# Kernel tuning notes

Measured on AMD Instinct MI355X. Metric: run time of the kernel, lower is better.

Reference implementation:

```python
import jax, jax.numpy as jnp
import numpy as np

B, M, N, P, H = 8192, 4, 2, 2, 128
D5 = M * 5            # FC5 output = m * in_mult_KNet
D2H = (H + H) * 40    # FC2 hidden = d_input_FC2 * out_mult_KNet


def _lin(x, W, b):
    return x @ W.T + b


def _gru(x, h, Wih, Whh, bih, bhh):
    # PyTorch GRU cell math (single layer, single step)
    gi = x @ Wih.T + bih   # [B, 3H]
    gh = h @ Whh.T + bhh   # [B, 3H]
    ir, iz, inn = jnp.split(gi, 3, axis=-1)
    hr, hz, hn = jnp.split(gh, 3, axis=-1)
    r = jax.nn.sigmoid(ir + hr)
    z = jax.nn.sigmoid(iz + hz)
    n = jnp.tanh(inn + r * hn)
    return (1.0 - z) * n + z * h


def setup_inputs() -> dict:
    key = jax.random.key(0)
    ks = iter(jax.random.split(key, 64))
    rn = lambda *s: jax.random.normal(next(ks), s, dtype=jnp.float32)
    sc = lambda d: np.float32(1.0 / np.sqrt(d))
    inp = {
        'y': rn(B, N, 1), 'u': rn(B, P, 1), 'm1x_post': rn(B, M, 1),
        'h_Q': jnp.zeros((B, H), jnp.float32),
        'h_Sigma': jnp.zeros((B, H), jnp.float32),
        'h_S': jnp.zeros((B, H), jnp.float32),
        'F_mat': jnp.eye(M, dtype=jnp.float32) + 0.1 * rn(M, M),
        'G_mat': 0.1 * rn(M, P),
        'H_mat': 0.5 * rn(N, M),
        'innov_logit': jnp.float32(0.0),
        'W_fc5': rn(D5, M) * sc(M), 'b_fc5': rn(D5) * 0.01,
        'Wih_Q': rn(3 * H, D5) * sc(H), 'Whh_Q': rn(3 * H, H) * sc(H),
        'bih_Q': rn(3 * H) * 0.01, 'bhh_Q': rn(3 * H) * 0.01,
        'Wih_Sig': rn(3 * H, H) * sc(H), 'Whh_Sig': rn(3 * H, H) * sc(H),
        'bih_Sig': rn(3 * H) * 0.01, 'bhh_Sig': rn(3 * H) * 0.01,
        'W_fc1': rn(N * N, H) * sc(H), 'b_fc1': rn(N * N) * 0.01,
        'W_fc7': rn(N, N) * sc(N), 'b_fc7': rn(N) * 0.01,
        'Wih_S': rn(3 * H, N * N + N) * sc(H), 'Whh_S': rn(3 * H, H) * sc(H),
        'bih_S': rn(3 * H) * 0.01, 'bhh_S': rn(3 * H) * 0.01,
        'W_fc2a': rn(D2H, 2 * H) * sc(2 * H), 'b_fc2a': rn(D2H) * 0.01,
        'W_fc2b': rn(N * M, D2H) * sc(D2H), 'b_fc2b': rn(N * M) * 0.01,
        'W_fc3': rn(M * M, H + N * M) * sc(H + N * M), 'b_fc3': rn(M * M) * 0.01,
        'W_fc4': rn(H, H + M * M) * sc(H + M * M), 'b_fc4': rn(H) * 0.01,
    }
    return inp


def reference(y, u, m1x_post, h_Q, h_Sigma, h_S, F_mat, G_mat, H_mat, innov_logit,
              W_fc5, b_fc5, Wih_Q, Whh_Q, bih_Q, bhh_Q,
              Wih_Sig, Whh_Sig, bih_Sig, bhh_Sig,
              W_fc1, b_fc1, W_fc7, b_fc7,
              Wih_S, Whh_S, bih_S, bhh_S,
              W_fc2a, b_fc2a, W_fc2b, b_fc2b,
              W_fc3, b_fc3, W_fc4, b_fc4):
    relu = jax.nn.relu
    # --- step_prior: linear system model f(x,u)=Fx+Gu, h(x)=Hx (no normalization) ---
    x_post = m1x_post[..., 0]                      # [B, M]
    x_prior = x_post @ F_mat.T + u[..., 0] @ G_mat.T
    y_pred = x_prior @ H_mat.T                     # [B, N]
    dy = y[..., 0] - y_pred                        # innovation [B, N]
    # --- KGain_step (dropout = identity at inference) ---
    out5 = relu(_lin(x_prior, W_fc5, b_fc5))       # [B, 20]
    hQ_new = _gru(out5, h_Q, Wih_Q, Whh_Q, bih_Q, bhh_Q)
    hSig = _gru(hQ_new, h_Sigma, Wih_Sig, Whh_Sig, bih_Sig, bhh_Sig)
    out1 = relu(_lin(hSig, W_fc1, b_fc1))          # [B, n^2]
    out7 = relu(_lin(dy, W_fc7, b_fc7))            # [B, n]
    hS_new = _gru(jnp.concatenate([out1, out7], -1), h_S, Wih_S, Whh_S, bih_S, bhh_S)
    in2 = jnp.concatenate([hSig, hS_new], -1)      # [B, 256]
    out2 = _lin(relu(_lin(in2, W_fc2a, b_fc2a)), W_fc2b, b_fc2b)  # KG flat [B, n*m]
    out3 = relu(_lin(jnp.concatenate([hS_new, out2], -1), W_fc3, b_fc3))
    hSig_new = relu(_lin(jnp.concatenate([hSig, out3], -1), W_fc4, b_fc4))
    # --- posterior update ---
    KG = out2.reshape(B, M, N)
    gamma = jax.nn.sigmoid(innov_logit)
    inov = gamma * jnp.einsum('bmn,bn->bm', KG, dy)
    m1x_posterior = (x_prior + inov)[..., None]    # [B, M, 1]
    return m1x_posterior, hQ_new, hSig_new, hS_new
```

## Files before the change

### kernel.cpp

```cpp
#include <hip/hip_runtime.h>
#include <hip/hip_bf16.h>

typedef __attribute__((ext_vector_type(8))) short bf16x8;
typedef __attribute__((ext_vector_type(4))) float f32x4;
typedef __attribute__((ext_vector_type(4))) short s16x4;
typedef __attribute__((ext_vector_type(4))) float f32v4;
typedef unsigned short u16;
typedef unsigned int u32;

__device__ inline u16 f2b(float f){ __hip_bfloat16 b = __float2bfloat16(f); return __builtin_bit_cast(unsigned short, b); }
__device__ inline float b2f(u16 u){ unsigned int x = ((unsigned int)u)<<16; return __builtin_bit_cast(float, x); }
__device__ inline float sigm(float x){ return 1.f/(1.f+__expf(-x)); }
__device__ inline float tanhfast(float x){ float e = __expf(2.f*x); return 1.f - 2.f/(e+1.f); }

__device__ inline f32x4 mfma16(bf16x8 a, bf16x8 b, f32x4 c){
  return __builtin_amdgcn_mfma_f32_16x16x32_bf16(a, b, c, 0, 0, 0);
}

__device__ __forceinline__ void in2t_store(u16* t, int row, int col, u16 v){
  int rt = row>>4, kk = col>>5, khi = (col>>3)&3, e = col&7;
  t[(size_t)(rt*8+kk)*512 + (khi*16 + (row&15))*8 + e] = v;
}
__device__ __forceinline__ s16x4 in2t_load4(const u16* t, int row, int col){
  int rt = row>>4, kk = col>>5, khi = (col>>3)&3, e = col&7;
  return *(const s16x4*)(t + (size_t)(rt*8+kk)*512 + (khi*16 + (row&15))*8 + e);
}

struct CVA {
  const float *w2a, *w2b, *wihQ, *whhQ, *wihSg, *whhSg, *wihS, *whhS, *wfc3, *wfc4;
  u16 *waB, *wbB, *wihQp, *whhQb, *wihSgB, *whhSgB, *wihSp, *whhSb, *wfc3p, *wfc4p;
};

__global__ __launch_bounds__(256) void kconv(CVA a){
  int id = blockIdx.x*256 + threadIdx.x;
  if (id < 2621440){
    int t  = id >> 12;
    int r  = id & 4095;
    int kk = r >> 9;
    int l  = (r >> 3) & 63;
    int e  = id & 7;
    int col = t*16 + (l & 15);
    int k   = kk*32 + (l >> 4)*8 + e;
    a.waB[id] = f2b(a.w2a[col*256 + k]);
    return;
  }
  id -= 2621440;
  if (id < 163840){
    int s = id >> 9;
    int r = id & 511;
    int l = r >> 3;
    int e = r & 7;
    int o = l & 15;
    int q = (l >> 4)*8 + e;
    int k = s*32 + (q&1)*16 + (q>>1);
    a.wbB[id] = (o < 8) ? f2b(a.w2b[o*10240 + k]) : (u16)0;
    return;
  }
  id -= 163840;
  if (id < 12288){ int j=id>>5, k=id&31; a.wihQp[id] = (k<20)? f2b(a.wihQ[j*20+k]) : (u16)0; return; }
  id -= 12288;
  if (id < 49152){ a.whhQb[id] = f2b(a.whhQ[id]); return; }
  id -= 49152;
  if (id < 49152){ a.wihSgB[id] = f2b(a.wihSg[id]); return; }
  id -= 49152;
  if (id < 49152){ a.whhSgB[id] = f2b(a.whhSg[id]); return; }
  id -= 49152;
  if (id < 12288){ int j=id>>5, k=id&31; a.wihSp[id] = (k<6)? f2b(a.wihS[j*6+k]) : (u16)0; return; }
  id -= 12288;
  if (id < 49152){ a.whhSb[id] = f2b(a.whhS[id]); return; }
  id -= 49152;
  if (id < 2560){ int j=id/160, k=id%160; a.wfc3p[id] = (k<136)? f2b(a.wfc3[j*136+k]) : (u16)0; return; }
}

__global__ __launch_bounds__(256) void kconv_fc4(const float* wfc4, u16* wfc4p){
  int id = blockIdx.x*256 + threadIdx.x;
  if (id < 20480){ int j=id/160, k=id%160; wfc4p[id] = (k<144)? f2b(wfc4[j*144+k]) : (u16)0; }
}

template<int KX, int LDX, bool SOUT, bool GB16, bool GF32>
__device__ __forceinline__ void gru_step(
    const u16* sX, const u16* sH,
    const u16* __restrict__ Wih, const int ldwih, const u16* __restrict__ Whh,
    const float* __restrict__ bih, const float* __restrict__ bhh,
    float* __restrict__ gOutF, u16* sOut,
    u16* __restrict__ in2T, int row0, int colOff)
{
  const int tid = threadIdx.x;
  const int w = tid>>6, lane = tid&63, c = lane&15, khi = lane>>4;
  for (int nn=0; nn<2; ++nn){
    const int n = w*2+nn;
    const int j = n*16 + c;
    const float bir=bih[j], biz=bih[128+j], bin=bih[256+j];
    const float bhr=bhh[j], bhz=bhh[128+j], bhn=bhh[256+j];
    bf16x8 BX0[KX], BX1[KX], BX2[KX], BH0[4], BH1[4], BH2[4];
    #pragma unroll
    for (int kk=0;kk<KX;++kk){
      const u16* p = Wih + j*ldwih + kk*32 + khi*8;
      BX0[kk] = *(const bf16x8*)(p);
      BX1[kk] = *(const bf16x8*)(p + 128*ldwih);
      BX2[kk] = *(const bf16x8*)(p + 256*ldwih);
    }
    #pragma unroll
    for (int kk=0;kk<4;++kk){
      const u16* p = Whh + j*128 + kk*32 + khi*8;
      BH0[kk] = *(const bf16x8*)(p);
      BH1[kk] = *(const bf16x8*)(p + 128*128);
      BH2[kk] = *(const bf16x8*)(p + 256*128);
    }
    #pragma unroll
    for (int m=0;m<2;++m){
      f32x4 ir={0,0,0,0}, iz={0,0,0,0}, inx={0,0,0,0};
      f32x4 hr={0,0,0,0}, hz={0,0,0,0}, hn={0,0,0,0};
      #pragma unroll
      for (int kk=0;kk<KX;++kk){
        bf16x8 A = *(const bf16x8*)(sX + (m*16+c)*LDX + kk*32 + khi*8);
        ir  = mfma16(A, BX0[kk], ir);
        iz  = mfma16(A, BX1[kk], iz);
        inx = mfma16(A, BX2[kk], inx);
      }
      #pragma unroll
      for (int kk=0;kk<4;++kk){
        bf16x8 A = *(const bf16x8*)(sH + (m*16+c)*136 + kk*32 + khi*8);
        hr = mfma16(A, BH0[kk], hr);
        hz = mfma16(A, BH1[kk], hz);
        hn = mfma16(A, BH2[kk], hn);
      }
      #pragma unroll
      for (int e=0;e<4;++e){
        int r = m*16 + khi*4 + e;
        float rg = sigm(ir[e]+hr[e]+bir+bhr);
        float zg = sigm(iz[e]+hz[e]+biz+bhz);
        float ng = tanhfast(inx[e]+bin + rg*(hn[e]+bhn));
        float hold = b2f(sH[r*136 + j]);
        float hv = (1.f-zg)*ng + zg*hold;
        if (GF32) gOutF[r*128 + j] = hv;
        if (SOUT) sOut[r*136 + j] = f2b(hv);
        if (GB16) in2t_store(in2T, row0 + r, colOff + j, f2b(hv));
      }
    }
  }
}

struct K1A {
  const float *y,*u,*m1x,*hQ,*hSg,*hS,*F,*G,*Hm,*W5,*b5,
              *bihQ,*bhhQ,*bihSg,*bhhSg,*W1,*b1,*W7,*b7,*bihS,*bhhS;
  const u16 *wihQp,*whhQ,*wihSg,*whhSg,*wihSp,*whhS;
  float *outHQ,*outHS,*xp,*dy;
  u16 *in2T;
};

__device__ __forceinline__ void load_h_tile(u16* dst, const float* src, int row0){
  const int tid = threadIdx.x;
  #pragma unroll
  for (int i=0;i<4;++i){
    int f4 = tid + i*256;
    int r = f4>>5, c4 = f4&31;
    f32v4 v = *(const f32v4*)(src + (row0+r)*128 + c4*4);
    s16x4 o;
    o[0]=(short)f2b(v[0]); o[1]=(short)f2b(v[1]);
    o[2]=(short)f2b(v[2]); o[3]=(short)f2b(v[3]);
    *(s16x4*)(dst + r*136 + c4*4) = o;
  }
}

__global__ __launch_bounds__(256) void k1(K1A a){
  __shared__ u16 sX[32*40];
  __shared__ u16 sH[32*136];
  __shared__ u16 sXL[32*136];
  __shared__ u16 sSig[32*136];
  __shared__ float sDY[64];
  const int row0 = blockIdx.x*32;
  const int tid = threadIdx.x;

  load_h_tile(sH, a.hQ, row0);
  if (tid < 32){
    int r = tid, row = row0 + r;
    float xpost[4], uu[2], xpr[4];
    #pragma unroll
    for (int i=0;i<4;++i) xpost[i]=a.m1x[row*4+i];
    uu[0]=a.u[row*2]; uu[1]=a.u[row*2+1];
    #pragma unroll
    for (int i=0;i<4;++i){
      float s=0.f;
      #pragma unroll
      for (int jj=0;jj<4;++jj) s += a.F[i*4+jj]*xpost[jj];
      #pragma unroll
      for (int jj=0;jj<2;++jj) s += a.G[i*2+jj]*uu[jj];
      xpr[i]=s; a.xp[row*4+i]=s;
    }
    #pragma unroll
    for (int nn2=0;nn2<2;++nn2){
      float s=0.f;
      #pragma unroll
      for (int jj=0;jj<4;++jj) s += a.Hm[nn2*4+jj]*xpr[jj];
      float d = a.y[row*2+nn2]-s;
      a.dy[row*2+nn2]=d; sDY[r*2+nn2]=d;
    }
    #pragma unroll
    for (int o=0;o<20;++o){
      float s=a.b5[o];
      #pragma unroll
      for (int k=0;k<4;++k) s += a.W5[o*4+k]*xpr[k];
      sX[r*40+o]=f2b(fmaxf(s,0.f));
    }
    for (int o=20;o<40;++o) sX[r*40+o]=0;
  }
  __syncthreads();
  gru_step<1,40,true,false,true>(sX, sH, a.wihQp, 32, a.whhQ, a.bihQ, a.bhhQ,
                                 a.outHQ + row0*128, sXL, nullptr, 0, 0);
  __syncthreads();
  load_h_tile(sH, a.hSg, row0);
  __syncthreads();
  gru_step<4,136,true,true,false>(sXL, sH, a.wihSg, 128, a.whhSg, a.bihSg, a.bhhSg,
                                  nullptr, sSig, a.in2T, row0, 0);
  __syncthreads();
  if (tid < 128){
    int r = tid>>2, o = tid&3;
    float s = a.b1[o];
    for (int k=0;k<128;++k) s += a.W1[o*128+k]*b2f(sSig[r*136+k]);
    sX[r*40+o] = f2b(fmaxf(s,0.f));
  } else if (tid < 192){
    int t = tid-128; int r=t>>1, o=t&1;
    float s = a.b7[o] + a.W7[o*2]*sDY[r*2] + a.W7[o*2+1]*sDY[r*2+1];
    sX[r*40+4+o] = f2b(fmaxf(s,0.f));
  }
  for (int i=tid;i<32*26;i+=256){ int r=i/26, cc=6+(i%26); sX[r*40+cc]=0; }
  load_h_tile(sH, a.hS, row0);
  __syncthreads();
  gru_step<1,40,false,true,true>(sX, sH, a.wihSp, 32, a.whhS, a.bihS, a.bhhS,
                                 a.outHS + row0*128, nullptr, a.in2T, row0, 128);
}

struct K2A {
  const u16 *waB, *wbB, *in2T;
  const float *b2a;
  float *parts;
};

__global__ __launch_bounds__(512) void k2(K2A a){
  __shared__ u16 sA[128*256];
  __shared__ u16 sHw[8][16*40];
  const int bid = blockIdx.x;
  const int rb = bid>>3, ch = bid&7;
  const int tid = threadIdx.x;
  const int wid = tid>>6, lane = tid&63, c = lane&15, khi = lane>>4;
  const int wr = wid>>2, wc = wid&3;

  {
    const s16x4* src = (const s16x4*)(a.in2T + (size_t)rb*32768);
    s16x4* dst = (s16x4*)sA;
    #pragma unroll
    for (int i=0;i<16;++i) dst[tid + i*512] = src[tid + i*512];
  }
  __syncthreads();

  f32x4 C2[4];
  #pragma unroll
  for (int m=0;m<4;++m) C2[m] = (f32x4){0,0,0,0};
  u16* hw = &sHw[wid][0];

  for (int it=0; it<10; ++it){
    const int colb = ch*1280 + it*128 + wc*32;
    const int t0 = colb>>4;
    f32x4 C1[4][2];
    #pragma unroll
    for (int m=0;m<4;++m){ C1[m][0]=(f32x4){0,0,0,0}; C1[m][1]=(f32x4){0,0,0,0}; }
    #pragma unroll
    for (int kk=0;kk<8;++kk){
      bf16x8 Bf0 = *(const bf16x8*)(a.waB + (size_t)(t0*8+kk)*512 + lane*8);
      bf16x8 Bf1 = *(const bf16x8*)(a.waB + (size_t)((t0+1)*8+kk)*512 + lane*8);
      #pragma unroll
      for (int m=0;m<4;++m){
        bf16x8 Ar = *(const bf16x8*)(sA + (size_t)((wr*4+m)*8+kk)*512 + lane*8);
        C1[m][0] = mfma16(Ar, Bf0, C1[m][0]);
        C1[m][1] = mfma16(Ar, Bf1, C1[m][1]);
      }
    }
    bf16x8 B2 = *(const bf16x8*)(a.wbB + (size_t)(colb>>5)*512 + lane*8);
    const float bias0 = a.b2a[colb + c];
    const float bias1 = a.b2a[colb + 16 + c];
    #pragma unroll
    for (int m=0;m<4;++m){
      #pragma unroll
      for (int e=0;e<4;++e){
        float v0 = fmaxf(C1[m][0][e]+bias0, 0.f);
        float v1 = fmaxf(C1[m][1][e]+bias1, 0.f);
        u32 w = (u32)f2b(v0) | ((u32)f2b(v1)<<16);
        *(u32*)(hw + (khi*4+e)*40 + 2*c) = w;
      }
      bf16x8 A2 = *(const bf16x8*)(hw + c*40 + khi*8);
      C2[m] = mfma16(A2, B2, C2[m]);
    }
  }
  __syncthreads();
  float* sRed = (float*)sA;
  if (c < 8){
    #pragma unroll
    for (int m=0;m<4;++m)
      #pragma unroll
      for (int e=0;e<4;++e)
        sRed[wid*512 + (m*16+khi*4+e)*8 + c] = C2[m][e];
  }
  __syncthreads();
  #pragma unroll
  for (int i=tid;i<1024;i+=512){
    int r=i>>3, o=i&7;
    int band=r>>6, rl=r&63;
    float s=0.f;
    #pragma unroll
    for (int w2=0;w2<4;++w2) s += sRed[(band*4+w2)*512 + rl*8 + o];
    a.parts[(size_t)ch*65536 + (size_t)(rb*128+r)*8 + o] = s;
  }
}

struct K3A {
  const float *parts;
  const float *b2b, *bfc3, *bfc4, *xp, *dy, *innov;
  const u16 *in2T, *wfc3p, *wfc4p;
  float *outPost, *outHSig;
};

__global__ __launch_bounds__(256) void k3(K3A a){
  __shared__ u16 sA[64*168];
  __shared__ u16 sX4[64*168];
  __shared__ float sOut2[64*8];
  const int row0 = blockIdx.x*64;
  const int tid = threadIdx.x;
  for (int i=tid;i<512;i+=256){
    int r=i>>3, o=i&7, row=row0+r;
    float s = a.b2b[o];
    #pragma unroll
    for (int chv=0;chv<8;++chv) s += a.parts[chv*65536 + row*8 + o];
    sOut2[i]=s;
    sA[r*168+128+o]=f2b(s);
  }
  for (int i=tid;i<2048;i+=256){
    int r=i>>5, c4=i&31;
    int row = row0 + r, col = c4*4;
    *(s16x4*)(sX4 + r*168 + col) = in2t_load4(a.in2T, row, col);
    *(s16x4*)(sA  + r*168 + col) = in2t_load4(a.in2T, row, 128 + col);
  }
  for (int i=tid;i<64*6;i+=256){
    int r=i/6, c4=i%6;
    *(s16x4*)(sA + r*168 + 136 + c4*4) = (s16x4){0,0,0,0};
  }
  for (int i=tid;i<64*4;i+=256){
    int r=i>>2, c4=i&3;
    *(s16x4*)(sX4 + r*168 + 144 + c4*4) = (s16x4){0,0,0,0};
  }
  __syncthreads();
  {
    int r = tid>>2, m = tid&3, row = row0+r;
    float g = 1.f/(1.f+__expf(-a.innov[0]));
    float d0 = a.dy[row*2], d1 = a.dy[row*2+1];
    float k0 = sOut2[r*8+m*2], k1 = sOut2[r*8+m*2+1];
    a.outPost[row*4+m] = a.xp[row*4+m] + g*(k0*d0+k1*d1);
  }
  const int w = tid>>6, lane = tid&63, c = lane&15, khi = lane>>4;
  {
    f32x4 C3 = {0,0,0,0};
    #pragma unroll
    for (int kk=0;kk<5;++kk){
      bf16x8 A  = *(const bf16x8*)(sA + (w*16+c)*168 + kk*32 + khi*8);
      bf16x8 Bf = *(const bf16x8*)(a.wfc3p + c*160 + kk*32 + khi*8);
      C3 = mfma16(A,Bf,C3);
    }
    float bj = a.bfc3[c];
    #pragma unroll
    for (int e=0;e<4;++e){
      int r = w*16 + khi*4 + e;
      sX4[r*168 + 128 + c] = f2b(fmaxf(C3[e]+bj, 0.f));
    }
  }
  __syncthreads();
  for (int nn=0;nn<2;++nn){
    int j = (w*2+nn)*16 + c;
    bf16x8 Bf[5];
    #pragma unroll
    for (int kk=0;kk<5;++kk) Bf[kk] = *(const bf16x8*)(a.wfc4p + j*160 + kk*32 + khi*8);
    float bj = a.bfc4[j];
    #pragma unroll
    for (int m=0;m<4;++m){
      f32x4 C = {0,0,0,0};
      #pragma unroll
      for (int kk=0;kk<5;++kk){
        bf16x8 A = *(const bf16x8*)(sX4 + (m*16+c)*168 + kk*32 + khi*8);
        C = mfma16(A, Bf[kk], C);
      }
      #pragma unroll
      for (int e=0;e<4;++e){
        int r = m*16 + khi*4 + e;
        a.outHSig[(row0+r)*128 + j] = fmaxf(C[e]+bj, 0.f);
      }
    }
  }
}

extern "C" void kernel_launch(void* const* d_in, const int* in_sizes, int n_in,
                              void* d_out, int out_size, void* d_ws, size_t ws_size,
                              hipStream_t stream){
  const float* y    = (const float*)d_in[0];
  const float* u    = (const float*)d_in[1];
  const float* m1x  = (const float*)d_in[2];
  const float* hQ   = (const float*)d_in[3];
  const float* hSg  = (const float*)d_in[4];
  const float* hS   = (const float*)d_in[5];
  const float* F    = (const float*)d_in[6];
  const float* G    = (const float*)d_in[7];
  const float* Hm   = (const float*)d_in[8];
  const float* innov= (const float*)d_in[9];
  const float* W5   = (const float*)d_in[10];
  const float* b5   = (const float*)d_in[11];
  const float* WihQ = (const float*)d_in[12];
  const float* WhhQ = (const float*)d_in[13];
  const float* bihQ = (const float*)d_in[14];
  const float* bhhQ = (const float*)d_in[15];
  const float* WihSg= (const float*)d_in[16];
  const float* WhhSg= (const float*)d_in[17];
  const float* bihSg= (const float*)d_in[18];
  const float* bhhSg= (const float*)d_in[19];
  const float* W1   = (const float*)d_in[20];
  const float* b1   = (const float*)d_in[21];
  const float* W7   = (const float*)d_in[22];
  const float* b7   = (const float*)d_in[23];
  const float* WihS = (const float*)d_in[24];
  const float* WhhS = (const float*)d_in[25];
  const float* bihS = (const float*)d_in[26];
  const float* bhhS = (const float*)d_in[27];
  const float* W2a  = (const float*)d_in[28];
  const float* b2a  = (const float*)d_in[29];
  const float* W2b  = (const float*)d_in[30];
  const float* b2b  = (const float*)d_in[31];
  const float* W3   = (const float*)d_in[32];
  const float* b3   = (const float*)d_in[33];
  const float* W4   = (const float*)d_in[34];
  const float* b4   = (const float*)d_in[35];

  const size_t WS_NEEDED = 12547072;
  if (ws_size < WS_NEEDED) return;

  char* ws = (char*)d_ws;
  u16*  waB   = (u16*)(ws + 0);
  u16*  wbB   = (u16*)(ws + 5242880);
  u16*  in2T  = (u16*)(ws + 5570560);
  float* parts= (float*)(ws + 9764864);
  float* xp   = (float*)(ws + 11862016);
  float* dyb  = (float*)(ws + 11993088);
  u16* wihQp  = (u16*)(ws + 12058624);
  u16* whhQb  = (u16*)(ws + 12083200);
  u16* wihSgB = (u16*)(ws + 12181504);
  u16* whhSgB = (u16*)(ws + 12279808);
  u16* wihSp  = (u16*)(ws + 12378112);
  u16* whhSb  = (u16*)(ws + 12402688);
  u16* wfc3p  = (u16*)(ws + 12500992);
  u16* wfc4p  = (u16*)(ws + 12506112);

  float* outF    = (float*)d_out;
  float* outPost = outF;
  float* outHQ   = outF + 32768;
  float* outHSig = outF + 32768 + 1048576;
  float* outHS   = outF + 32768 + 2*1048576;

  CVA cv{W2a, W2b, WihQ, WhhQ, WihSg, WhhSg, WihS, WhhS, W3, W4,
         waB, wbB, wihQp, whhQb, wihSgB, whhSgB, wihSp, whhSb, wfc3p, wfc4p};
  kconv<<<dim3(11834), dim3(256), 0, stream>>>(cv);
  kconv_fc4<<<dim3(80), dim3(256), 0, stream>>>(W4, wfc4p);

  K1A a1{y,u,m1x,hQ,hSg,hS,F,G,Hm,W5,b5,bihQ,bhhQ,bihSg,bhhSg,W1,b1,W7,b7,bihS,bhhS,
         wihQp,whhQb,wihSgB,whhSgB,wihSp,whhSb,
         outHQ,outHS,xp,dyb,in2T};
  k1<<<dim3(256), dim3(256), 0, stream>>>(a1);

  K2A a2{waB, wbB, in2T, b2a, parts};
  k2<<<dim3(512), dim3(512), 0, stream>>>(a2);

  K3A a3{parts, b2b, b3, b4, xp, dyb, innov, in2T, wfc3p, wfc4p, outPost, outHSig};
  k3<<<dim3(128), dim3(256), 0, stream>>>(a3);
}
```

Before: 100.8 us.

## Vectorize weight conversion, merge fc4 conversion, MFMA fc1, halve k3 tile

The weight-conversion kernel now handles eight elements per thread with float4 loads for the large FC2 weights, and the separate fc4 conversion launch is folded into it. This cuts thread count and one launch. In k1 the scalar 128-length fc1 dot products are replaced by a single-wave MFMA, and the zero-fill is spread across the remaining waves. k3 now processes 32 rows per block over 256 blocks to improve occupancy, at the cost of idle waves during the fc3 stage.

```diff
diff --git a/kernel.cpp b/kernel.cpp
--- a/kernel.cpp
+++ b/kernel.cpp
@@ -33,30 +33,44 @@
 
 __global__ __launch_bounds__(256) void kconv(CVA a){
   int id = blockIdx.x*256 + threadIdx.x;
-  if (id < 2621440){
-    int t  = id >> 12;
-    int r  = id & 4095;
-    int kk = r >> 9;
-    int l  = (r >> 3) & 63;
-    int e  = id & 7;
-    int col = t*16 + (l & 15);
-    int k   = kk*32 + (l >> 4)*8 + e;
-    a.waB[id] = f2b(a.w2a[col*256 + k]);
+  if (id < 327680){
+    int g = id >> 6;
+    int l = id & 63;
+    int col = (g>>3)*16 + (l & 15);
+    int k0  = (g&7)*32 + (l >> 4)*8;
+    const float* p = a.w2a + (size_t)col*256 + k0;
+    f32v4 v0 = *(const f32v4*)p;
+    f32v4 v1 = *(const f32v4*)(p+4);
+    s16x4 o0, o1;
+    #pragma unroll
+    for (int e=0;e<4;++e){ o0[e]=(short)f2b(v0[e]); o1[e]=(short)f2b(v1[e]); }
+    u16* d = a.waB + (size_t)g*512 + l*8;
+    *(s16x4*)d = o0; *(s16x4*)(d+4) = o1;
     return;
   }
-  id -= 2621440;
-  if (id < 163840){
-    int s = id >> 9;
-    int r = id & 511;
-    int l = r >> 3;
-    int e = r & 7;
+  id -= 327680;
+  if (id < 20480){
+    int l = id & 63;
     int o = l & 15;
-    int q = (l >> 4)*8 + e;
-    int k = s*32 + (q&1)*16 + (q>>1);
-    a.wbB[id] = (o < 8) ? f2b(a.w2b[o*10240 + k]) : (u16)0;
+    int b = (l >> 4)*4;
+    u16* d = a.wbB + (size_t)id*8;
+    if (o < 8){
+      int s = id >> 6;
+      const float* p = a.w2b + (size_t)o*10240 + s*32;
+      f32v4 v0 = *(const f32v4*)(p + b);
+      f32v4 v1 = *(const f32v4*)(p + 16 + b);
+      s16x4 o0, o1;
+      o0[0]=(short)f2b(v0[0]); o0[1]=(short)f2b(v1[0]);
+      o0[2]=(short)f2b(v0[1]); o0[3]=(short)f2b(v1[1]);
+      o1[0]=(short)f2b(v0[2]); o1[1]=(short)f2b(v1[2]);
+      o1[2]=(short)f2b(v0[3]); o1[3]=(short)f2b(v1[3]);
+      *(s16x4*)d = o0; *(s16x4*)(d+4) = o1;
+    } else {
+      *(s16x4*)d = (s16x4){0,0,0,0}; *(s16x4*)(d+4) = (s16x4){0,0,0,0};
+    }
     return;
   }
-  id -= 163840;
+  id -= 20480;
   if (id < 12288){ int j=id>>5, k=id&31; a.wihQp[id] = (k<20)? f2b(a.wihQ[j*20+k]) : (u16)0; return; }
   id -= 12288;
   if (id < 49152){ a.whhQb[id] = f2b(a.whhQ[id]); return; }
@@ -70,11 +84,8 @@
   if (id < 49152){ a.whhSb[id] = f2b(a.whhS[id]); return; }
   id -= 49152;
   if (id < 2560){ int j=id/160, k=id%160; a.wfc3p[id] = (k<136)? f2b(a.wfc3[j*136+k]) : (u16)0; return; }
-}
-
-__global__ __launch_bounds__(256) void kconv_fc4(const float* wfc4, u16* wfc4p){
-  int id = blockIdx.x*256 + threadIdx.x;
-  if (id < 20480){ int j=id/160, k=id%160; wfc4p[id] = (k<144)? f2b(wfc4[j*144+k]) : (u16)0; }
+  id -= 2560;
+  if (id < 20480){ int j=id/160, k=id%160; a.wfc4p[id] = (k<144)? f2b(a.wfc4[j*144+k]) : (u16)0; return; }
 }
 
 template<int KX, int LDX, bool SOUT, bool GB16, bool GF32>
@@ -171,6 +182,7 @@
   __shared__ float sDY[64];
   const int row0 = blockIdx.x*32;
   const int tid = threadIdx.x;
+  const int wid = tid>>6, lane = tid&63, c = lane&15, khi = lane>>4;
 
   load_h_tile(sH, a.hQ, row0);
   if (tid < 32){
@@ -214,17 +226,44 @@
   gru_step<4,136,true,true,false>(sXL, sH, a.wihSg, 128, a.whhSg, a.bihSg, a.bhhSg,
                                   nullptr, sSig, a.in2T, row0, 0);
   __syncthreads();
-  if (tid < 128){
-    int r = tid>>2, o = tid&3;
-    float s = a.b1[o];
-    for (int k=0;k<128;++k) s += a.W1[o*128+k]*b2f(sSig[r*136+k]);
-    sX[r*40+o] = f2b(fmaxf(s,0.f));
-  } else if (tid < 192){
-    int t = tid-128; int r=t>>1, o=t&1;
+  if (wid == 0){
+    bf16x8 Bf[4];
+    #pragma unroll
+    for (int kk=0;kk<4;++kk){
+      bf16x8 b = (bf16x8){0,0,0,0,0,0,0,0};
+      if (c < 4){
+        const float* p = a.W1 + c*128 + kk*32 + khi*8;
+        f32v4 v0 = *(const f32v4*)p;
+        f32v4 v1 = *(const f32v4*)(p+4);
+        #pragma unroll
+        for (int e=0;e<4;++e){ b[e]=(short)f2b(v0[e]); b[4+e]=(short)f2b(v1[e]); }
+      }
+      Bf[kk] = b;
+    }
+    float bj = (c < 4) ? a.b1[c] : 0.f;
+    #pragma unroll
+    for (int m=0;m<2;++m){
+      f32x4 C = {0,0,0,0};
+      #pragma unroll
+      for (int kk=0;kk<4;++kk){
+        bf16x8 A = *(const bf16x8*)(sSig + (m*16+c)*136 + kk*32 + khi*8);
+        C = mfma16(A, Bf[kk], C);
+      }
+      if (c < 4){
+        #pragma unroll
+        for (int e=0;e<4;++e){
+          int r = m*16 + khi*4 + e;
+          sX[r*40 + c] = f2b(fmaxf(C[e]+bj, 0.f));
+        }
+      }
+    }
+  } else if (wid == 1){
+    int r = lane>>1, o = lane&1;
     float s = a.b7[o] + a.W7[o*2]*sDY[r*2] + a.W7[o*2+1]*sDY[r*2+1];
     sX[r*40+4+o] = f2b(fmaxf(s,0.f));
-  }
-  for (int i=tid;i<32*26;i+=256){ int r=i/26, cc=6+(i%26); sX[r*40+cc]=0; }
+  } else {
+    for (int i=tid-128;i<832;i+=128){ int r=i/26, cc=6+(i%26); sX[r*40+cc]=0; }
+  }
   load_h_tile(sH, a.hS, row0);
   __syncthreads();
   gru_step<1,40,false,true,true>(sX, sH, a.wihSp, 32, a.whhS, a.bihS, a.bhhS,
@@ -321,35 +360,29 @@
 };
 
 __global__ __launch_bounds__(256) void k3(K3A a){
-  __shared__ u16 sA[64*168];
-  __shared__ u16 sX4[64*168];
-  __shared__ float sOut2[64*8];
-  const int row0 = blockIdx.x*64;
+  __shared__ u16 sA[32*168];
+  __shared__ u16 sX4[32*168];
+  __shared__ float sOut2[32*8];
+  const int row0 = blockIdx.x*32;
   const int tid = threadIdx.x;
-  for (int i=tid;i<512;i+=256){
-    int r=i>>3, o=i&7, row=row0+r;
+  {
+    int r=tid>>3, o=tid&7, row=row0+r;
     float s = a.b2b[o];
     #pragma unroll
     for (int chv=0;chv<8;++chv) s += a.parts[chv*65536 + row*8 + o];
-    sOut2[i]=s;
+    sOut2[tid]=s;
     sA[r*168+128+o]=f2b(s);
   }
-  for (int i=tid;i<2048;i+=256){
+  for (int i=tid;i<1024;i+=256){
     int r=i>>5, c4=i&31;
     int row = row0 + r, col = c4*4;
     *(s16x4*)(sX4 + r*168 + col) = in2t_load4(a.in2T, row, col);
     *(s16x4*)(sA  + r*168 + col) = in2t_load4(a.in2T, row, 128 + col);
   }
-  for (int i=tid;i<64*6;i+=256){
-    int r=i/6, c4=i%6;
-    *(s16x4*)(sA + r*168 + 136 + c4*4) = (s16x4){0,0,0,0};
-  }
-  for (int i=tid;i<64*4;i+=256){
-    int r=i>>2, c4=i&3;
-    *(s16x4*)(sX4 + r*168 + 144 + c4*4) = (s16x4){0,0,0,0};
-  }
-  __syncthreads();
-  {
+  if (tid < 192){ int r=tid/6, c4=tid%6; *(s16x4*)(sA + r*168 + 136 + c4*4) = (s16x4){0,0,0,0}; }
+  if (tid < 128){ int r=tid>>2, c4=tid&3; *(s16x4*)(sX4 + r*168 + 144 + c4*4) = (s16x4){0,0,0,0}; }
+  __syncthreads();
+  if (tid < 128){
     int r = tid>>2, m = tid&3, row = row0+r;
     float g = 1.f/(1.f+__expf(-a.innov[0]));
     float d0 = a.dy[row*2], d1 = a.dy[row*2+1];
@@ -357,7 +390,7 @@
     a.outPost[row*4+m] = a.xp[row*4+m] + g*(k0*d0+k1*d1);
   }
   const int w = tid>>6, lane = tid&63, c = lane&15, khi = lane>>4;
-  {
+  if (w < 2){
     f32x4 C3 = {0,0,0,0};
     #pragma unroll
     for (int kk=0;kk<5;++kk){
@@ -380,7 +413,7 @@
     for (int kk=0;kk<5;++kk) Bf[kk] = *(const bf16x8*)(a.wfc4p + j*160 + kk*32 + khi*8);
     float bj = a.bfc4[j];
     #pragma unroll
-    for (int m=0;m<4;++m){
+    for (int m=0;m<2;++m){
       f32x4 C = {0,0,0,0};
       #pragma unroll
       for (int kk=0;kk<5;++kk){
@@ -463,8 +496,7 @@
 
   CVA cv{W2a, W2b, WihQ, WhhQ, WihSg, WhhSg, WihS, WhhS, W3, W4,
          waB, wbB, wihQp, whhQb, wihSgB, whhSgB, wihSp, whhSb, wfc3p, wfc4p};
-  kconv<<<dim3(11834), dim3(256), 0, stream>>>(cv);
-  kconv_fc4<<<dim3(80), dim3(256), 0, stream>>>(W4, wfc4p);
+  kconv<<<dim3(2314), dim3(256), 0, stream>>>(cv);
 
   K1A a1{y,u,m1x,hQ,hSg,hS,F,G,Hm,W5,b5,bihQ,bhhQ,bihSg,bhhSg,W1,b1,W7,b7,bihS,bhhS,
          wihQp,whhQb,wihSgB,whhSgB,wihSp,whhSb,
@@ -475,5 +507,5 @@
   k2<<<dim3(512), dim3(512), 0, stream>>>(a2);
 
   K3A a3{parts, b2b, b3, b4, xp, dyb, innov, in2T, wfc3p, wfc4p, outPost, outHSig};
-  k3<<<dim3(128), dim3(256), 0, stream>>>(a3);
-}
+  k3<<<dim3(256), dim3(256), 0, stream>>>(a3);
+}
```

Result: faster. 93.02 us (-7.7%).
